# Optimization experiments

Measured on AMD Instinct MI355X. Metric: run time of the kernel, lower is better.

The kernel has to match this reference:

```python
import jax, jax.numpy as jnp
import numpy as np

EMBED_DIM = 128
NUM_CLASSES = 2
NUM_NODES = 100000
NUM_EDGES = 500000


def setup_inputs() -> dict:
    key = jax.random.key(0)
    k1, k2, k3, k4, k5, k6 = jax.random.split(key, 6)
    node_embed = jax.random.normal(k1, (NUM_NODES, EMBED_DIM), dtype=jnp.float32)
    edge_index = jax.random.randint(k2, (2, NUM_EDGES), 0, NUM_NODES, dtype=jnp.int64)
    # MLP params (torch Linear default init scale ~ 1/sqrt(fan_in))
    s1 = 1.0 / np.sqrt(2 * EMBED_DIM)
    s2 = 1.0 / np.sqrt(EMBED_DIM)
    W1 = jax.random.uniform(k3, (2 * EMBED_DIM, EMBED_DIM), jnp.float32, -s1, s1)
    b1 = jax.random.uniform(k4, (EMBED_DIM,), jnp.float32, -s1, s1)
    W2 = jax.random.uniform(k5, (EMBED_DIM, NUM_CLASSES), jnp.float32, -s2, s2)
    b2 = jax.random.uniform(k6, (NUM_CLASSES,), jnp.float32, -s2, s2)
    return {"node_embed": node_embed, "edge_index": edge_index,
            "W1": W1, "b1": b1, "W2": W2, "b2": b2}


def reference(node_embed, edge_index, W1, b1, W2, b2):
    row, col = edge_index[0], edge_index[1]
    # Gather endpoint embeddings and concat -> [num_edges, 2*embed_dim]
    edge_feat = jnp.concatenate([node_embed[row], node_embed[col]], axis=1)
    h = jax.nn.relu(edge_feat @ W1 + b1)  # [num_edges, embed_dim]
    # Dropout(0.1) is identity in eval mode.
    return h @ W2 + b2  # [num_edges, num_classes]
```

## Files before the change

### kernel.cpp

```cpp
#include <hip/hip_runtime.h>
#include <hip/hip_bf16.h>


#define EMBED 128

typedef _Float16 half8 __attribute__((ext_vector_type(8)));
typedef _Float16 half4 __attribute__((ext_vector_type(4)));
typedef float floatx4 __attribute__((ext_vector_type(4)));

__global__ __launch_bounds__(256) void prep(
    const float* __restrict__ W1, const float* __restrict__ W2,
    const float* __restrict__ b1, const int* __restrict__ idx,
    _Float16* __restrict__ WT, _Float16* __restrict__ W2PT,
    _Float16* __restrict__ b1f, int* __restrict__ flag) {
    if (blockIdx.x < 128) {
        __shared__ float lds[16][17];
        const int ty = threadIdx.x >> 4, tx = threadIdx.x & 15;
        const int r0 = (blockIdx.x >> 3) * 16;
        const int c0 = (blockIdx.x & 7) * 16;
        lds[ty][tx] = W1[(r0 + ty) * 128 + c0 + tx];
        __syncthreads();
        const int jbase = c0 + (r0 >= 128 ? 128 : 0);
        const int kbase = r0 & 127;
        WT[(size_t)(jbase + ty) * 128 + kbase + tx] = (_Float16)lds[tx][ty];
    } else {
        const int t = threadIdx.x;
        if (t < 64) {
            const int hw = idx[2 * t + 1];
            const unsigned long long m = __ballot(hw != 0);
            if (t == 0) *flag = (m == 0ull) ? 1 : 0;
        }
        if (t < 128) b1f[t] = (_Float16)b1[t];
        for (int i = t; i < 2048; i += 256) {
            const int n = i >> 7, k = i & 127;
            W2PT[i] = (n < 2) ? (_Float16)W2[k * 2 + n] : (_Float16)0.f;
        }
    }
}

__global__ __launch_bounds__(256) void gemm_ab(
    const float* __restrict__ X, const _Float16* __restrict__ WT,
    _Float16* __restrict__ AB, int n_nodes, int n_tiles) {
    __shared__ _Float16 sh[64 * 264];
    _Float16* xs   = sh;
    _Float16* outs = sh;
    const int t = threadIdx.x;
    const int w = t >> 6, lane = t & 63, lm = lane & 15, quad = lane >> 4;

    int srow[8], scol[8];
#pragma unroll
    for (int i = 0; i < 8; ++i) {
        const int flat = i * 1024 + t * 4;
        srow[i] = flat >> 7;
        scol[i] = flat & 127;
    }

    int T = blockIdx.x;
    float4 pf[8];
    if (T < n_tiles) {
#pragma unroll
        for (int i = 0; i < 8; ++i) {
            int node = T * 64 + srow[i];
            if (node > n_nodes - 1) node = n_nodes - 1;
            pf[i] = *(const float4*)(X + (size_t)node * EMBED + scol[i]);
        }
    }

    for (; T < n_tiles; T += gridDim.x) {
        const int mblk = T * 64;

#pragma unroll
        for (int i = 0; i < 8; ++i) {
            half4 h;
            h[0] = (_Float16)pf[i].x; h[1] = (_Float16)pf[i].y;
            h[2] = (_Float16)pf[i].z; h[3] = (_Float16)pf[i].w;
            *(half4*)(xs + srow[i] * 136 + scol[i]) = h;
        }
        __syncthreads();

        const int Tn = T + gridDim.x;
        if (Tn < n_tiles) {
#pragma unroll
            for (int i = 0; i < 8; ++i) {
                int node = Tn * 64 + srow[i];
                if (node > n_nodes - 1) node = n_nodes - 1;
                pf[i] = *(const float4*)(X + (size_t)node * EMBED + scol[i]);
            }
        }

        floatx4 acc[4][4];
#pragma unroll
        for (int a = 0; a < 4; ++a)
#pragma unroll
            for (int b = 0; b < 4; ++b)
                acc[a][b] = (floatx4){0.f, 0.f, 0.f, 0.f};

#pragma unroll
        for (int ks = 0; ks < 4; ++ks) {
            const int k0 = ks * 32 + quad * 8;
            half8 xf[4];
#pragma unroll
            for (int mf = 0; mf < 4; ++mf)
                xf[mf] = *(const half8*)(xs + (mf * 16 + lm) * 136 + k0);
#pragma unroll
            for (int jf = 0; jf < 4; ++jf) {
                const int j = w * 64 + jf * 16 + lm;
                const half8 wf = *(const half8*)(WT + (size_t)j * EMBED + k0);
#pragma unroll
                for (int mf = 0; mf < 4; ++mf)
                    acc[mf][jf] = __builtin_amdgcn_mfma_f32_16x16x32_f16(wf, xf[mf], acc[mf][jf], 0, 0, 0);
            }
        }
        __syncthreads();

#pragma unroll
        for (int mf = 0; mf < 4; ++mf) {
#pragma unroll
            for (int jf = 0; jf < 4; ++jf) {
                half4 h;
#pragma unroll
                for (int r = 0; r < 4; ++r) h[r] = (_Float16)acc[mf][jf][r];
                *(half4*)(outs + (mf * 16 + lm) * 264 + w * 64 + jf * 16 + quad * 4) = h;
            }
        }
        __syncthreads();

#pragma unroll
        for (int i = 0; i < 8; ++i) {
            const int idx8 = i * 256 + t;
            const int node = idx8 >> 5, jj = idx8 & 31;
            if (mblk + node < n_nodes)
                *(half8*)(AB + (size_t)(mblk + node) * 256 + jj * 8) =
                    *(const half8*)(outs + node * 264 + jj * 8);
        }
        __syncthreads();
    }
}

__global__ __launch_bounds__(256) void edge_mlp(
    const _Float16* __restrict__ AB, const int* __restrict__ eidx,
    const int* __restrict__ flag, const _Float16* __restrict__ b1f,
    const _Float16* __restrict__ W2PT, const float* __restrict__ b2,
    float* __restrict__ out, int n_edges) {
    const int lane = threadIdx.x & 63, lm = lane & 15, quad = lane >> 4;
    const int ebase = (blockIdx.x * 4 + (threadIdx.x >> 6)) * 32;
    if (ebase >= n_edges) return;

    const int mode = *flag;
    int e0 = ebase + lm, e1 = ebase + 16 + lm;
    if (e0 > n_edges - 1) e0 = n_edges - 1;
    if (e1 > n_edges - 1) e1 = n_edges - 1;
    int row0, col0, row1, col1;
    if (mode) {
        row0 = eidx[2 * (size_t)e0];
        col0 = eidx[2 * ((size_t)n_edges + e0)];
        row1 = eidx[2 * (size_t)e1];
        col1 = eidx[2 * ((size_t)n_edges + e1)];
    } else {
        row0 = eidx[e0];
        col0 = eidx[(size_t)n_edges + e0];
        row1 = eidx[e1];
        col1 = eidx[(size_t)n_edges + e1];
    }

    const _Float16* a0p = AB + (size_t)row0 * 256;
    const _Float16* b0p = AB + (size_t)col0 * 256 + 128;
    const _Float16* a1p = AB + (size_t)row1 * 256;
    const _Float16* b1p = AB + (size_t)col1 * 256 + 128;

    half8 a0[4], b0[4], a1[4], b1[4];
#pragma unroll
    for (int ks = 0; ks < 4; ++ks) {
        const int k0 = ks * 32 + quad * 8;
        a0[ks] = *(const half8*)(a0p + k0);
        b0[ks] = *(const half8*)(b0p + k0);
        a1[ks] = *(const half8*)(a1p + k0);
        b1[ks] = *(const half8*)(b1p + k0);
    }

    floatx4 acc0 = (floatx4){0.f, 0.f, 0.f, 0.f};
    floatx4 acc1 = (floatx4){0.f, 0.f, 0.f, 0.f};
#pragma unroll
    for (int ks = 0; ks < 4; ++ks) {
        const int k0 = ks * 32 + quad * 8;
        const half8 bi = *(const half8*)(b1f + k0);
        const half8 wv = *(const half8*)(W2PT + lm * 128 + k0);
        half8 h0 = a0[ks] + b0[ks] + bi;
        half8 h1 = a1[ks] + b1[ks] + bi;
#pragma unroll
        for (int j = 0; j < 8; ++j) {
            h0[j] = h0[j] > (_Float16)0.f ? h0[j] : (_Float16)0.f;
            h1[j] = h1[j] > (_Float16)0.f ? h1[j] : (_Float16)0.f;
        }
        acc0 = __builtin_amdgcn_mfma_f32_16x16x32_f16(h0, wv, acc0, 0, 0, 0);
        acc1 = __builtin_amdgcn_mfma_f32_16x16x32_f16(h1, wv, acc1, 0, 0, 0);
    }

    if (lm < 2) {
        const float b2v = b2[lm];
#pragma unroll
        for (int r = 0; r < 4; ++r) {
            const int ed0 = ebase + quad * 4 + r;
            const int ed1 = ebase + 16 + quad * 4 + r;
            if (ed0 < n_edges) out[(size_t)ed0 * 2 + lm] = acc0[r] + b2v;
            if (ed1 < n_edges) out[(size_t)ed1 * 2 + lm] = acc1[r] + b2v;
        }
    }
}

extern "C" void kernel_launch(void* const* d_in, const int* in_sizes, int n_in,
                              void* d_out, int out_size, void* d_ws, size_t ws_size,
                              hipStream_t stream) {
    const float* X   = (const float*)d_in[0];
    const int*   idx = (const int*)d_in[1];
    const float* W1  = (const float*)d_in[2];
    const float* b1  = (const float*)d_in[3];
    const float* W2  = (const float*)d_in[4];
    const float* b2  = (const float*)d_in[5];
    float* out = (float*)d_out;

    const int n_nodes = in_sizes[0] / EMBED;
    const int n_edges = in_sizes[1] / 2;

    char* ws = (char*)d_ws;
    int*      flag = (int*)ws;
    _Float16* AB   = (_Float16*)(ws + 256);
    _Float16* WT   = (_Float16*)(ws + 256 + (size_t)n_nodes * 512);
    _Float16* W2PT = WT + 256 * 128;
    _Float16* b1f  = W2PT + 16 * 128;

    const int n_tiles = (n_nodes + 63) / 64;

    prep<<<129, 256, 0, stream>>>(W1, W2, b1, idx, WT, W2PT, b1f, flag);
    gemm_ab<<<782, 256, 0, stream>>>(X, WT, AB, n_nodes, n_tiles);
    edge_mlp<<<(n_edges + 127) / 128, 256, 0, stream>>>(
        AB, idx, flag, b1f, W2PT, b2, out, n_edges);
}
```

Baseline: 154.2 us.

## Bucket edges by source node range for L2 locality in edge MLP

Adds a partition kernel that groups edges into 8 buckets by source-node range and writes (row, col, edge) records, so each group of edge_mlp blocks works on one bucket. The aim is to keep the row-side half of the AB table for one node range resident in cache (one slice per XCD, assuming round-robin block placement), cutting random gather traffic. edge_mlp becomes a persistent grid-stride kernel with hoisted weight loads and scatters outputs through shuffled edge ids. The cost is an extra kernel launch, global atomics and a record write/read pass, and the column gathers stay random.

```diff
diff --git a/kernel.cpp b/kernel.cpp
--- a/kernel.cpp
+++ b/kernel.cpp
@@ -7,12 +7,14 @@
 typedef _Float16 half8 __attribute__((ext_vector_type(8)));
 typedef _Float16 half4 __attribute__((ext_vector_type(4)));
 typedef float floatx4 __attribute__((ext_vector_type(4)));
+typedef int intx4 __attribute__((ext_vector_type(4)));
 
 __global__ __launch_bounds__(256) void prep(
     const float* __restrict__ W1, const float* __restrict__ W2,
     const float* __restrict__ b1, const int* __restrict__ idx,
     _Float16* __restrict__ WT, _Float16* __restrict__ W2PT,
-    _Float16* __restrict__ b1f, int* __restrict__ flag) {
+    _Float16* __restrict__ b1f, int* __restrict__ flag,
+    int* __restrict__ bcnt) {
     if (blockIdx.x < 128) {
         __shared__ float lds[16][17];
         const int ty = threadIdx.x >> 4, tx = threadIdx.x & 15;
@@ -30,11 +32,44 @@
             const unsigned long long m = __ballot(hw != 0);
             if (t == 0) *flag = (m == 0ull) ? 1 : 0;
         }
+        if (t < 8) bcnt[t] = 0;
         if (t < 128) b1f[t] = (_Float16)b1[t];
         for (int i = t; i < 2048; i += 256) {
             const int n = i >> 7, k = i & 127;
             W2PT[i] = (n < 2) ? (_Float16)W2[k * 2 + n] : (_Float16)0.f;
         }
+    }
+}
+
+__global__ __launch_bounds__(256) void partition(
+    const int* __restrict__ eidx, const int* __restrict__ flag,
+    int* __restrict__ bcnt, int* __restrict__ recs, int cap,
+    int n_edges, int n_nodes) {
+    __shared__ int lcnt[8], lbase[8];
+    const int t = threadIdx.x;
+    const int mode = *flag;
+    const unsigned bsize = (unsigned)(n_nodes + 7) / 8u;
+    for (int base = blockIdx.x * 256; base < n_edges; base += gridDim.x * 256) {
+        const int e = base + t;
+        int r = 0, c = 0, b = 0;
+        const bool act = e < n_edges;
+        if (act) {
+            r = eidx[(size_t)e << mode];
+            c = eidx[((size_t)n_edges + e) << mode];
+            b = (int)((unsigned)r / bsize);
+        }
+        if (t < 8) lcnt[t] = 0;
+        __syncthreads();
+        int myoff = 0;
+        if (act) myoff = atomicAdd(&lcnt[b], 1);
+        __syncthreads();
+        if (t < 8) lbase[t] = atomicAdd(&bcnt[t], lcnt[t]);
+        __syncthreads();
+        if (act) {
+            const size_t p = (size_t)b * cap + lbase[b] + myoff;
+            *(intx4*)(recs + p * 4) = (intx4){r, c, e, 0};
+        }
+        __syncthreads();
     }
 }
 
@@ -137,73 +172,76 @@
     }
 }
 
-__global__ __launch_bounds__(256) void edge_mlp(
-    const _Float16* __restrict__ AB, const int* __restrict__ eidx,
-    const int* __restrict__ flag, const _Float16* __restrict__ b1f,
-    const _Float16* __restrict__ W2PT, const float* __restrict__ b2,
-    float* __restrict__ out, int n_edges) {
+__global__ __launch_bounds__(256, 3) void edge_mlp(
+    const _Float16* __restrict__ AB, const int* __restrict__ recs,
+    const int* __restrict__ bcnt, int cap,
+    const _Float16* __restrict__ b1f, const _Float16* __restrict__ W2PT,
+    const float* __restrict__ b2, float* __restrict__ out) {
     const int lane = threadIdx.x & 63, lm = lane & 15, quad = lane >> 4;
-    const int ebase = (blockIdx.x * 4 + (threadIdx.x >> 6)) * 32;
-    if (ebase >= n_edges) return;
-
-    const int mode = *flag;
-    int e0 = ebase + lm, e1 = ebase + 16 + lm;
-    if (e0 > n_edges - 1) e0 = n_edges - 1;
-    if (e1 > n_edges - 1) e1 = n_edges - 1;
-    int row0, col0, row1, col1;
-    if (mode) {
-        row0 = eidx[2 * (size_t)e0];
-        col0 = eidx[2 * ((size_t)n_edges + e0)];
-        row1 = eidx[2 * (size_t)e1];
-        col1 = eidx[2 * ((size_t)n_edges + e1)];
-    } else {
-        row0 = eidx[e0];
-        col0 = eidx[(size_t)n_edges + e0];
-        row1 = eidx[e1];
-        col1 = eidx[(size_t)n_edges + e1];
-    }
-
-    const _Float16* a0p = AB + (size_t)row0 * 256;
-    const _Float16* b0p = AB + (size_t)col0 * 256 + 128;
-    const _Float16* a1p = AB + (size_t)row1 * 256;
-    const _Float16* b1p = AB + (size_t)col1 * 256 + 128;
-
-    half8 a0[4], b0[4], a1[4], b1[4];
+    const int bkt = blockIdx.x & 7;
+    const int wslot = (blockIdx.x >> 3) * 4 + (threadIdx.x >> 6);
+    const int WPB = (gridDim.x >> 3) * 4;
+    const int cnt = bcnt[bkt];
+    if (cnt == 0) return;
+    const int G = (cnt + 15) >> 4;
+    const int* rb = recs + (size_t)bkt * cap * 4;
+
+    const float b2v = b2[lm & 1];
+
+    half8 wv[4], bvv[4];
 #pragma unroll
     for (int ks = 0; ks < 4; ++ks) {
-        const int k0 = ks * 32 + quad * 8;
-        a0[ks] = *(const half8*)(a0p + k0);
-        b0[ks] = *(const half8*)(b0p + k0);
-        a1[ks] = *(const half8*)(a1p + k0);
-        b1[ks] = *(const half8*)(b1p + k0);
-    }
-
-    floatx4 acc0 = (floatx4){0.f, 0.f, 0.f, 0.f};
-    floatx4 acc1 = (floatx4){0.f, 0.f, 0.f, 0.f};
-#pragma unroll
-    for (int ks = 0; ks < 4; ++ks) {
-        const int k0 = ks * 32 + quad * 8;
-        const half8 bi = *(const half8*)(b1f + k0);
-        const half8 wv = *(const half8*)(W2PT + lm * 128 + k0);
-        half8 h0 = a0[ks] + b0[ks] + bi;
-        half8 h1 = a1[ks] + b1[ks] + bi;
-#pragma unroll
-        for (int j = 0; j < 8; ++j) {
-            h0[j] = h0[j] > (_Float16)0.f ? h0[j] : (_Float16)0.f;
-            h1[j] = h1[j] > (_Float16)0.f ? h1[j] : (_Float16)0.f;
-        }
-        acc0 = __builtin_amdgcn_mfma_f32_16x16x32_f16(h0, wv, acc0, 0, 0, 0);
-        acc1 = __builtin_amdgcn_mfma_f32_16x16x32_f16(h1, wv, acc1, 0, 0, 0);
-    }
-
-    if (lm < 2) {
-        const float b2v = b2[lm];
+        wv[ks]  = *(const half8*)(W2PT + lm * 128 + ks * 32 + quad * 8);
+        bvv[ks] = *(const half8*)(b1f + ks * 32 + quad * 8);
+    }
+
+    for (int g0 = 2 * wslot; g0 < G; g0 += 2 * WPB) {
+        const int g1 = g0 + 1;
+        int p0 = g0 * 16 + lm; p0 = p0 < cnt ? p0 : cnt - 1;
+        int p1 = g1 * 16 + lm; p1 = p1 < cnt ? p1 : cnt - 1;
+        const intx4 rec0 = *(const intx4*)(rb + (size_t)p0 * 4);
+        const intx4 rec1 = *(const intx4*)(rb + (size_t)p1 * 4);
+
+        const _Float16* a0p = AB + (size_t)(unsigned)rec0[0] * 256 + quad * 8;
+        const _Float16* b0p = AB + (size_t)(unsigned)rec0[1] * 256 + 128 + quad * 8;
+        const _Float16* a1p = AB + (size_t)(unsigned)rec1[0] * 256 + quad * 8;
+        const _Float16* b1p = AB + (size_t)(unsigned)rec1[1] * 256 + 128 + quad * 8;
+        half8 d0[8], d1[8];
+#pragma unroll
+        for (int ks = 0; ks < 4; ++ks) {
+            d0[ks]     = *(const half8*)(a0p + ks * 32);
+            d0[ks + 4] = *(const half8*)(b0p + ks * 32);
+            d1[ks]     = *(const half8*)(a1p + ks * 32);
+            d1[ks + 4] = *(const half8*)(b1p + ks * 32);
+        }
+
+        floatx4 acc0 = (floatx4){0.f, 0.f, 0.f, 0.f};
+        floatx4 acc1 = (floatx4){0.f, 0.f, 0.f, 0.f};
+#pragma unroll
+        for (int ks = 0; ks < 4; ++ks) {
+            half8 h0 = d0[ks] + d0[ks + 4] + bvv[ks];
+            half8 h1 = d1[ks] + d1[ks + 4] + bvv[ks];
+#pragma unroll
+            for (int j = 0; j < 8; ++j) {
+                h0[j] = h0[j] > (_Float16)0.f ? h0[j] : (_Float16)0.f;
+                h1[j] = h1[j] > (_Float16)0.f ? h1[j] : (_Float16)0.f;
+            }
+            acc0 = __builtin_amdgcn_mfma_f32_16x16x32_f16(h0, wv[ks], acc0, 0, 0, 0);
+            acc1 = __builtin_amdgcn_mfma_f32_16x16x32_f16(h1, wv[ks], acc1, 0, 0, 0);
+        }
+
+        const int ez0 = rec0[2], ez1 = rec1[2];
 #pragma unroll
         for (int r = 0; r < 4; ++r) {
-            const int ed0 = ebase + quad * 4 + r;
-            const int ed1 = ebase + 16 + quad * 4 + r;
-            if (ed0 < n_edges) out[(size_t)ed0 * 2 + lm] = acc0[r] + b2v;
-            if (ed1 < n_edges) out[(size_t)ed1 * 2 + lm] = acc1[r] + b2v;
+            const int src = quad * 4 + r;
+            const int i0 = __shfl(ez0, src, 64);
+            const int i1 = __shfl(ez1, src, 64);
+            if (lm < 2) {
+                if (g0 * 16 + src < cnt)
+                    out[(size_t)(unsigned)i0 * 2 + lm] = acc0[r] + b2v;
+                if (g1 * 16 + src < cnt)
+                    out[(size_t)(unsigned)i1 * 2 + lm] = acc1[r] + b2v;
+            }
         }
     }
 }
@@ -221,18 +259,25 @@
 
     const int n_nodes = in_sizes[0] / EMBED;
     const int n_edges = in_sizes[1] / 2;
+    const int cap = n_edges;
 
     char* ws = (char*)d_ws;
     int*      flag = (int*)ws;
+    int*      bcnt = (int*)(ws + 64);
     _Float16* AB   = (_Float16*)(ws + 256);
     _Float16* WT   = (_Float16*)(ws + 256 + (size_t)n_nodes * 512);
     _Float16* W2PT = WT + 256 * 128;
     _Float16* b1f  = W2PT + 16 * 128;
+    char* p = (char*)(b1f + 128);
+    p = (char*)(((uintptr_t)p + 255) & ~(uintptr_t)255);
+    int* recs = (int*)p;
 
     const int n_tiles = (n_nodes + 63) / 64;
 
-    prep<<<129, 256, 0, stream>>>(W1, W2, b1, idx, WT, W2PT, b1f, flag);
+    prep<<<129, 256, 0, stream>>>(W1, W2, b1, idx, WT, W2PT, b1f, flag, bcnt);
+    partition<<<256, 256, 0, stream>>>(idx, flag, bcnt, recs, cap,
+                                       n_edges, n_nodes);
     gemm_ab<<<782, 256, 0, stream>>>(X, WT, AB, n_nodes, n_tiles);
-    edge_mlp<<<(n_edges + 127) / 128, 256, 0, stream>>>(
-        AB, idx, flag, b1f, W2PT, b2, out, n_edges);
-}
+    edge_mlp<<<768, 256, 0, stream>>>(
+        AB, recs, bcnt, cap, b1f, W2PT, b2, out);
+}
```

Result: slower. 170.2 us (+10.4%).
